# Performance work log

Hardware: AMD Instinct MI355X
Metric: run time of the kernel (lower is better)

## Reference

```python
import jax, jax.numpy as jnp
import numpy as np

N_QUBITS = 14
N_LAYERS = 2          # n_ansatz_layers
N_TIMESTEPS = 4
DEGREE = 2
N_ROTS = 4 * N_QUBITS * N_LAYERS  # 448 rotation params per qnode call
DIM = 2 ** N_QUBITS
BSZ = 256
STATE_DIM = 4
OUT_DIM = 2


def apply_ry(state, wire, theta):
    # state: (B, 2^n) complex64; theta: (B,) float. Wire 0 = most significant bit (PennyLane convention).
    L, R = 2 ** wire, 2 ** (N_QUBITS - wire - 1)
    st = state.reshape(-1, L, 2, R)
    c = jnp.cos(theta * 0.5)[:, None, None]
    s = jnp.sin(theta * 0.5)[:, None, None]
    s0, s1 = st[:, :, 0, :], st[:, :, 1, :]
    new = jnp.stack([c * s0 - s * s1, s * s0 + c * s1], axis=2)
    return new.reshape(state.shape)


def apply_crx(state, ctrl, tgt, theta):
    # Controlled-RX: RX(theta) on tgt when ctrl bit is 1.
    a, b = (ctrl, tgt) if ctrl < tgt else (tgt, ctrl)
    La, Lm, Lr = 2 ** a, 2 ** (b - a - 1), 2 ** (N_QUBITS - b - 1)
    st = state.reshape(-1, La, 2, Lm, 2, Lr)
    c = jnp.cos(theta * 0.5)[:, None, None, None]
    s = jnp.sin(theta * 0.5)[:, None, None, None]
    if ctrl < tgt:
        # axis2 = ctrl, axis4 = tgt
        ctl1 = st[:, :, 1]                      # (B, La, Lm, 2, Lr)
        t0, t1 = ctl1[:, :, :, 0, :], ctl1[:, :, :, 1, :]
        n0 = c * t0 - 1j * s * t1
        n1 = -1j * s * t0 + c * t1
        new_ctl1 = jnp.stack([n0, n1], axis=3)
        out = jnp.stack([st[:, :, 0], new_ctl1], axis=2)
    else:
        # axis2 = tgt, axis4 = ctrl
        t0c1, t1c1 = st[:, :, 0, :, 1, :], st[:, :, 1, :, 1, :]
        n0 = c * t0c1 - 1j * s * t1c1
        n1 = -1j * s * t0c1 + c * t1c1
        new_t0 = jnp.stack([st[:, :, 0, :, 0, :], n0], axis=3)
        new_t1 = jnp.stack([st[:, :, 1, :, 0, :], n1], axis=3)
        out = jnp.stack([new_t0, new_t1], axis=2)
    return out.reshape(state.shape)


def sim14(state, params):
    # sim14_circuit: per layer -> RY ring, descending CRX ring [i,(i+1)%n], RY ring, CRX ring [i,(i-1)%n].
    idx = 0
    for _ in range(N_LAYERS):
        for i in range(N_QUBITS):
            state = apply_ry(state, i, params[:, idx]); idx += 1
        for i in range(N_QUBITS - 1, -1, -1):
            state = apply_crx(state, i, (i + 1) % N_QUBITS, params[:, idx]); idx += 1
        for i in range(N_QUBITS):
            state = apply_ry(state, i, params[:, idx]); idx += 1
        for i in [N_QUBITS - 1] + list(range(N_QUBITS - 1)):
            state = apply_crx(state, i, (i - 1) % N_QUBITS, params[:, idx]); idx += 1
    return state


def poly_state(base, tparams, mix_coeffs, poly_coeffs):
    # evaluate_polynomial_state_pl: degree+1 rounds of timestep-mixed circuit outputs.
    result = jnp.zeros_like(base)
    for d in range(DEGREE + 1):
        mixed = jnp.zeros_like(base)
        for t in range(N_TIMESTEPS):
            mixed = mixed + mix_coeffs[:, t:t + 1] * sim14(base, tparams[:, t, :])
        result = result + poly_coeffs[d] * mixed
        if d < DEGREE:
            nrm = jnp.linalg.norm(mixed, axis=1, keepdims=True)
            base = mixed / (nrm + 1e-9)
    return result


def expval_z(state, wire):
    L, R = 2 ** wire, 2 ** (N_QUBITS - wire - 1)
    st = state.reshape(-1, L, 2, R)
    p = jnp.sum(jnp.abs(st) ** 2, axis=(1, 3))  # (B, 2)
    return p[:, 0] - p[:, 1]


def setup_inputs() -> dict:
    key = jax.random.key(0)
    ks = jax.random.split(key, 7)
    return {
        "x": jax.random.normal(ks[0], (BSZ, STATE_DIM), dtype=jnp.float32),
        "W_in": jax.random.normal(ks[1], (STATE_DIM, N_TIMESTEPS * N_ROTS), dtype=jnp.float32) * 0.3,
        "b_in": jax.random.normal(ks[2], (N_TIMESTEPS * N_ROTS,), dtype=jnp.float32) * 0.1,
        "mix_coeffs": jax.random.normal(ks[3], (1, N_TIMESTEPS), dtype=jnp.float32) * 0.5,
        "poly_coeffs": jax.random.normal(ks[4], (DEGREE + 1,), dtype=jnp.float32) * 0.5,
        "W_out": jax.random.normal(ks[5], (N_QUBITS, OUT_DIM), dtype=jnp.float32) * 0.3,
        "b_out": jax.random.normal(ks[6], (OUT_DIM,), dtype=jnp.float32) * 0.1,
    }


def reference(x, W_in, b_in, mix_coeffs, poly_coeffs, W_out, b_out):
    bsz = x.shape[0]
    # v1-style sigmoid [0,1] angle scaling
    angles = jax.nn.sigmoid(x @ W_in + b_in)                # (B, T*n_rots)
    tparams = angles.reshape(bsz, N_TIMESTEPS, N_ROTS)
    base = jnp.zeros((bsz, DIM), dtype=jnp.complex64).at[:, 0].set(1.0)
    final = poly_state(base, tparams, mix_coeffs, poly_coeffs)
    final = final / (jnp.linalg.norm(final, axis=1, keepdims=True) + 1e-9)
    expz = jnp.stack([expval_z(final, w) for w in range(N_QUBITS)], axis=1)  # (B, n_qubits) real
    return expz.astype(jnp.float32) @ W_out + b_out
```

## Files before the change

### kernel.cpp

```cpp
#include <hip/hip_runtime.h>
#include <math.h>

#define DIM 16384
#define NTH 512

typedef float v2f __attribute__((ext_vector_type(2)));

__host__ __device__ constexpr int cswz(int i) {
  return i ^ ((i >> 4) & 15) ^ ((i >> 8) & 15) ^ ((i >> 12) & 3);
}

constexpr int LW[8][5] = {
  {13, 12, 11, 10, 0},
  {10, 9, 8, 7, 6},
  {6, 5, 4, 3, 2},
  {2, 1, 0, 3, 4},
  {12, 13, 0, 1, 2},
  {2, 3, 4, 5, 6},
  {6, 7, 8, 9, 10},
  {10, 11, 12, 13, 9},
};
constexpr int PMAP[8][9] = {
  {4, 5, 6, 7, 8, 9, 10, 11, 12},
  {0, 1, 2, 11, 8, 9, 10, 12, 13},
  {0, 1, 2, 3, 4, 5, 6, 12, 13},
  {0, 1, 2, 3, 4, 5, 6, 7, 8},
  {2, 3, 4, 5, 6, 7, 8, 9, 10},
  {0, 1, 2, 3, 4, 5, 6, 12, 13},
  {0, 1, 2, 11, 8, 9, 10, 12, 13},
  {5, 6, 7, 8, 9, 10, 11, 12, 13},
};
constexpr int NG[8] = {9, 8, 8, 3, 9, 8, 8, 3};
constexpr int GATES[8][9][4] = {
  {{0,4,0,0},{0,3,0,10},{0,2,0,11},{0,1,0,12},{0,0,0,13},{1,0,4,14},{1,1,0,15},{1,2,1,16},{1,3,2,17}},
  {{0,4,0,6},{0,3,0,7},{0,2,0,8},{0,1,0,9},{1,1,0,18},{1,2,1,19},{1,3,2,20},{1,4,3,21},{0,0,0,0}},
  {{0,4,0,2},{0,3,0,3},{0,2,0,4},{0,1,0,5},{1,1,0,22},{1,2,1,23},{1,3,2,24},{1,4,3,25},{0,0,0,0}},
  {{0,1,0,1},{1,1,0,26},{1,2,1,27},{0,0,0,0},{0,0,0,0},{0,0,0,0},{0,0,0,0},{0,0,0,0},{0,0,0,0}},
  {{0,2,0,28},{0,3,0,29},{0,4,0,30},{0,0,0,40},{0,1,0,41},{1,1,0,42},{1,2,1,43},{1,3,2,44},{1,4,3,45}},
  {{0,1,0,31},{0,2,0,32},{0,3,0,33},{0,4,0,34},{1,1,0,46},{1,2,1,47},{1,3,2,48},{1,4,3,49},{0,0,0,0}},
  {{0,1,0,35},{0,2,0,36},{0,3,0,37},{0,4,0,38},{1,1,0,50},{1,2,1,51},{1,3,2,52},{1,4,3,53},{0,0,0,0}},
  {{0,1,0,39},{1,1,0,54},{1,2,1,55},{0,0,0,0},{0,0,0,0},{0,0,0,0},{0,0,0,0},{0,0,0,0},{0,0,0,0}},
};

__host__ __device__ constexpr int offcube(int p, int j) {
  int o = 0;
  for (int b = 0; b < 5; ++b)
    if ((j >> b) & 1) o |= 1 << (13 - LW[p][b]);
  return o;
}

template <int PID, int MODE>
__device__ __forceinline__ void run_pass(v2f* __restrict__ S, const v2f* __restrict__ CS,
                                         int lb, int tid, v2f* __restrict__ a) {
  int base = 0;
#pragma unroll
  for (int k = 0; k < 9; ++k) base |= ((tid >> k) & 1) << PMAP[PID][k];
  const int sb = cswz(base);
  if (MODE == 1) {
#pragma unroll
    for (int j = 0; j < 32; ++j) a[j] = v2f{0.f, 0.f};
    if (tid == 0) a[0] = v2f{1.f, 0.f};
  } else {
#pragma unroll
    for (int j = 0; j < 32; ++j) a[j] = S[sb ^ cswz(offcube(PID, j))];
  }
#pragma unroll
  for (int g = 0; g < NG[PID]; ++g) {
    const v2f cs2 = CS[lb + GATES[PID][g][3]];
    const float c = cs2.x, s = cs2.y;
    if (GATES[PID][g][0] == 0) {
      const int tb = GATES[PID][g][1];
#pragma unroll
      for (int j = 0; j < 32; ++j)
        if (!((j >> tb) & 1)) {
          const int j2 = j | (1 << tb);
          const v2f a0 = a[j], a1 = a[j2];
          a[j]  = c * a0 - s * a1;
          a[j2] = s * a0 + c * a1;
        }
    } else {
      const int bc = GATES[PID][g][1], bt = GATES[PID][g][2];
#pragma unroll
      for (int j = 0; j < 32; ++j)
        if (((j >> bc) & 1) && !((j >> bt) & 1)) {
          const int j2 = j | (1 << bt);
          const v2f t0 = a[j], t1 = a[j2];
          a[j]  = c * t0 + s * v2f{t1.y, -t1.x};
          a[j2] = c * t1 + s * v2f{t0.y, -t0.x};
        }
    }
  }
  if (MODE != 2) {
#pragma unroll
    for (int j = 0; j < 32; ++j) S[sb ^ cswz(offcube(PID, j))] = a[j];
  }
  __syncthreads();
}

__device__ __forceinline__ void run_sim(v2f* __restrict__ S, const v2f* __restrict__ CS,
                                        int tid, v2f* __restrict__ a,
                                        const v2f* __restrict__ basev, int own_sb,
                                        bool initzero) {
  if (initzero) {
    run_pass<0, 1>(S, CS, 0, tid, a);
  } else {
#pragma unroll
    for (int j = 0; j < 32; ++j) S[own_sb ^ cswz(offcube(7, j))] = basev[j];
    __syncthreads();
    run_pass<0, 0>(S, CS, 0, tid, a);
  }
  run_pass<1, 0>(S, CS, 0, tid, a);
  run_pass<2, 0>(S, CS, 0, tid, a);
  run_pass<3, 0>(S, CS, 0, tid, a);
  run_pass<4, 0>(S, CS, 0, tid, a);
  run_pass<5, 0>(S, CS, 0, tid, a);
  run_pass<6, 0>(S, CS, 0, tid, a);
  run_pass<7, 0>(S, CS, 0, tid, a);
  run_pass<0, 0>(S, CS, 56, tid, a);
  run_pass<1, 0>(S, CS, 56, tid, a);
  run_pass<2, 0>(S, CS, 56, tid, a);
  run_pass<3, 0>(S, CS, 56, tid, a);
  run_pass<4, 0>(S, CS, 56, tid, a);
  run_pass<5, 0>(S, CS, 56, tid, a);
  run_pass<6, 0>(S, CS, 56, tid, a);
  run_pass<7, 2>(S, CS, 56, tid, a);
}

__device__ __forceinline__ float block_sum(float v, int tid, float* red) {
#pragma unroll
  for (int off = 32; off; off >>= 1) v += __shfl_xor(v, off);
  if ((tid & 63) == 0) red[tid >> 6] = v;
  __syncthreads();
  float tot = 0.f;
#pragma unroll
  for (int w = 0; w < 8; ++w) tot += red[w];
  __syncthreads();
  return tot;
}

__global__ void
__attribute__((amdgpu_flat_work_group_size(512, 512)))
__attribute__((amdgpu_waves_per_eu(2, 2)))
qts_kernel(
    const float* __restrict__ x, const float* __restrict__ Win,
    const float* __restrict__ bin, const float* __restrict__ mix,
    const float* __restrict__ poly, const float* __restrict__ Wout,
    const float* __restrict__ bout, float* __restrict__ out) {
  extern __shared__ v2f S[];
  v2f* CSall = S + DIM;
  float* red = (float*)(S + DIM + 448);
  const int tid = threadIdx.x;
  const int b = blockIdx.x;

  if (tid < 448) {
    float z = bin[tid];
    const float x0 = x[b * 4 + 0], x1 = x[b * 4 + 1], x2 = x[b * 4 + 2], x3 = x[b * 4 + 3];
    z += x0 * Win[tid] + x1 * Win[448 + tid] + x2 * Win[896 + tid] + x3 * Win[1344 + tid];
    const float th = 1.f / (1.f + expf(-z));
    float sn, cc;
    sincosf(0.5f * th, &sn, &cc);
    CSall[tid] = v2f{cc, sn};
  }
  __syncthreads();

  int ownbase = 0;
#pragma unroll
  for (int k = 0; k < 9; ++k) ownbase |= ((tid >> k) & 1) << PMAP[7][k];
  const int own_sb = cswz(ownbase);

  const float p0 = poly[0], p1 = poly[1], p2 = poly[2];

  v2f a[32], acc[32], basev[32];
  float alpha;

#pragma unroll
  for (int j = 0; j < 32; ++j) acc[j] = v2f{0.f, 0.f};
  for (int t = 0; t < 4; ++t) {
    run_sim(S, CSall + t * 112, tid, a, basev, own_sb, true);
    const float mc = mix[t];
#pragma unroll
    for (int j = 0; j < 32; ++j) acc[j] += mc * a[j];
  }
  {
    float part = 0.f;
#pragma unroll
    for (int j = 0; j < 32; ++j) part += acc[j].x * acc[j].x + acc[j].y * acc[j].y;
    const float tot = block_sum(part, tid, red);
    const float nu = sqrtf(tot) + 1e-9f;
    const float inv = 1.f / nu;
    alpha = p0 * nu;
#pragma unroll
    for (int j = 0; j < 32; ++j) { basev[j] = inv * acc[j]; acc[j] = v2f{0.f, 0.f}; }
  }

  for (int t = 0; t < 4; ++t) {
    run_sim(S, CSall + t * 112, tid, a, basev, own_sb, false);
    const float mc = mix[t];
#pragma unroll
    for (int j = 0; j < 32; ++j) acc[j] += mc * a[j];
  }
  {
    float part = 0.f;
#pragma unroll
    for (int j = 0; j < 32; ++j) part += acc[j].x * acc[j].x + acc[j].y * acc[j].y;
    const float tot = block_sum(part, tid, red);
    const float nu = sqrtf(tot) + 1e-9f;
    const float inv = 1.f / nu;
#pragma unroll
    for (int j = 0; j < 32; ++j) {
      const v2f tmp = acc[j];
      acc[j] = alpha * basev[j] + p1 * tmp;
      basev[j] = inv * tmp;
    }
  }

  for (int t = 0; t < 4; ++t) {
    run_sim(S, CSall + t * 112, tid, a, basev, own_sb, false);
    const float mc = p2 * mix[t];
#pragma unroll
    for (int j = 0; j < 32; ++j) acc[j] += mc * a[j];
  }

  float part[15];
#pragma unroll
  for (int v = 0; v < 15; ++v) part[v] = 0.f;
#pragma unroll
  for (int j = 0; j < 32; ++j) {
    const int idx = ownbase | offcube(7, j);
    const float p = acc[j].x * acc[j].x + acc[j].y * acc[j].y;
    part[14] += p;
#pragma unroll
    for (int w = 0; w < 14; ++w) part[w] += ((idx >> (13 - w)) & 1) ? -p : p;
  }
  __syncthreads();
#pragma unroll
  for (int v = 0; v < 15; ++v) {
    float xv = part[v];
#pragma unroll
    for (int off = 32; off; off >>= 1) xv += __shfl_xor(xv, off);
    if ((tid & 63) == 0) red[(tid >> 6) * 15 + v] = xv;
  }
  __syncthreads();
  if (tid < 15) {
    float tot = 0.f;
#pragma unroll
    for (int w = 0; w < 8; ++w) tot += red[w * 15 + tid];
    red[128 + tid] = tot;
  }
  __syncthreads();
  if (tid < 2) {
    const float nrm = sqrtf(red[128 + 14]) + 1e-9f;
    const float iv = 1.f / (nrm * nrm);
    float o = bout[tid];
#pragma unroll
    for (int w = 0; w < 14; ++w) o += red[128 + w] * iv * Wout[w * 2 + tid];
    out[b * 2 + tid] = o;
  }
}

extern "C" void kernel_launch(void* const* d_in, const int* in_sizes, int n_in,
                              void* d_out, int out_size, void* d_ws, size_t ws_size,
                              hipStream_t stream) {
  const float* x    = (const float*)d_in[0];
  const float* Win  = (const float*)d_in[1];
  const float* bin  = (const float*)d_in[2];
  const float* mix  = (const float*)d_in[3];
  const float* poly = (const float*)d_in[4];
  const float* Wout = (const float*)d_in[5];
  const float* bout = (const float*)d_in[6];
  float* out = (float*)d_out;

  const size_t shmem = (size_t)DIM * sizeof(v2f) + 448 * sizeof(v2f) + 1024;
  hipFuncSetAttribute((const void*)qts_kernel,
                      hipFuncAttributeMaxDynamicSharedMemorySize, (int)shmem);
  qts_kernel<<<256, NTH, shmem, stream>>>(x, Win, bin, mix, poly, Wout, bout, out);
}
```

Baseline: 945.7 us.

## Use 1024 threads with 16 amplitudes each and a 10-pass gate schedule

The block grows from 512 to 1024 threads. Each thread now holds 16 amplitudes over a 4-qubit local subcube instead of 32 over 5 qubits, and the gate schedule is regrouped into 10 passes per layer instead of 8. Per-pass base offsets are precomputed once into a register array. The aim is to cut register pressure and raise the number of waves hiding LDS latency, at the cost of more shared-memory passes and __syncthreads barriers per simulation.

```diff
diff --git a/kernel.cpp b/kernel.cpp
--- a/kernel.cpp
+++ b/kernel.cpp
@@ -2,7 +2,8 @@
 #include <math.h>
 
 #define DIM 16384
-#define NTH 512
+#define NTH 1024
+#define APT 16
 
 typedef float v2f __attribute__((ext_vector_type(2)));
 
@@ -10,68 +11,70 @@
   return i ^ ((i >> 4) & 15) ^ ((i >> 8) & 15) ^ ((i >> 12) & 3);
 }
 
-constexpr int LW[8][5] = {
-  {13, 12, 11, 10, 0},
-  {10, 9, 8, 7, 6},
-  {6, 5, 4, 3, 2},
-  {2, 1, 0, 3, 4},
-  {12, 13, 0, 1, 2},
-  {2, 3, 4, 5, 6},
-  {6, 7, 8, 9, 10},
-  {10, 11, 12, 13, 9},
+constexpr int LWp[10][4] = {
+  {13, 0, 12, 11},
+  {10, 9, 8, 11},
+  {7, 6, 5, 8},
+  {4, 3, 2, 5},
+  {1, 0, 2, 3},
+  {13, 12, 0, 1},
+  {2, 1, 3, 4},
+  {5, 4, 6, 7},
+  {8, 7, 9, 10},
+  {11, 10, 12, 9},
 };
-constexpr int PMAP[8][9] = {
-  {4, 5, 6, 7, 8, 9, 10, 11, 12},
-  {0, 1, 2, 11, 8, 9, 10, 12, 13},
-  {0, 1, 2, 3, 4, 5, 6, 12, 13},
-  {0, 1, 2, 3, 4, 5, 6, 7, 8},
-  {2, 3, 4, 5, 6, 7, 8, 9, 10},
-  {0, 1, 2, 3, 4, 5, 6, 12, 13},
-  {0, 1, 2, 11, 8, 9, 10, 12, 13},
-  {5, 6, 7, 8, 9, 10, 11, 12, 13},
+constexpr int PM[10][10] = {
+  {3, 4, 5, 6, 7, 8, 9, 10, 11, 12},
+  {0, 1, 6, 7, 8, 9, 10, 11, 12, 13},
+  {0, 1, 2, 3, 4, 9, 10, 11, 12, 13},
+  {0, 1, 2, 3, 4, 5, 6, 7, 12, 13},
+  {0, 1, 2, 3, 4, 5, 6, 7, 8, 9},
+  {2, 3, 4, 5, 6, 7, 8, 9, 10, 11},
+  {0, 1, 2, 3, 4, 5, 6, 7, 8, 13},
+  {0, 1, 2, 3, 4, 5, 10, 11, 12, 13},
+  {0, 1, 2, 7, 8, 9, 10, 11, 12, 13},
+  {0, 5, 6, 7, 8, 9, 10, 11, 12, 13},
 };
-constexpr int NG[8] = {9, 8, 8, 3, 9, 8, 8, 3};
-constexpr int GATES[8][9][4] = {
-  {{0,4,0,0},{0,3,0,10},{0,2,0,11},{0,1,0,12},{0,0,0,13},{1,0,4,14},{1,1,0,15},{1,2,1,16},{1,3,2,17}},
-  {{0,4,0,6},{0,3,0,7},{0,2,0,8},{0,1,0,9},{1,1,0,18},{1,2,1,19},{1,3,2,20},{1,4,3,21},{0,0,0,0}},
-  {{0,4,0,2},{0,3,0,3},{0,2,0,4},{0,1,0,5},{1,1,0,22},{1,2,1,23},{1,3,2,24},{1,4,3,25},{0,0,0,0}},
-  {{0,1,0,1},{1,1,0,26},{1,2,1,27},{0,0,0,0},{0,0,0,0},{0,0,0,0},{0,0,0,0},{0,0,0,0},{0,0,0,0}},
-  {{0,2,0,28},{0,3,0,29},{0,4,0,30},{0,0,0,40},{0,1,0,41},{1,1,0,42},{1,2,1,43},{1,3,2,44},{1,4,3,45}},
-  {{0,1,0,31},{0,2,0,32},{0,3,0,33},{0,4,0,34},{1,1,0,46},{1,2,1,47},{1,3,2,48},{1,4,3,49},{0,0,0,0}},
-  {{0,1,0,35},{0,2,0,36},{0,3,0,37},{0,4,0,38},{1,1,0,50},{1,2,1,51},{1,3,2,52},{1,4,3,53},{0,0,0,0}},
-  {{0,1,0,39},{1,1,0,54},{1,2,1,55},{0,0,0,0},{0,0,0,0},{0,0,0,0},{0,0,0,0},{0,0,0,0},{0,0,0,0}},
+constexpr int NGp[10] = {7, 6, 6, 6, 3, 7, 6, 6, 6, 3};
+constexpr int GT[10][7][4] = {
+  {{0,0,0,13},{0,1,0,0},{0,2,0,12},{0,3,0,11},{1,0,1,14},{1,2,0,15},{1,3,2,16}},
+  {{0,0,0,10},{0,1,0,9},{0,2,0,8},{1,0,3,17},{1,1,0,18},{1,2,1,19},{0,0,0,0}},
+  {{0,0,0,7},{0,1,0,6},{0,2,0,5},{1,0,3,20},{1,1,0,21},{1,2,1,22},{0,0,0,0}},
+  {{0,0,0,4},{0,1,0,3},{0,2,0,2},{1,0,3,23},{1,1,0,24},{1,2,1,25},{0,0,0,0}},
+  {{0,0,0,1},{1,0,2,26},{1,1,0,27},{0,0,0,0},{0,0,0,0},{0,0,0,0},{0,0,0,0}},
+  {{0,0,0,41},{0,1,0,40},{0,2,0,28},{0,3,0,29},{1,0,1,42},{1,2,0,43},{1,3,2,44}},
+  {{0,0,0,30},{0,2,0,31},{0,3,0,32},{1,0,1,45},{1,2,0,46},{1,3,2,47},{0,0,0,0}},
+  {{0,0,0,33},{0,2,0,34},{0,3,0,35},{1,0,1,48},{1,2,0,49},{1,3,2,50},{0,0,0,0}},
+  {{0,0,0,36},{0,2,0,37},{0,3,0,38},{1,0,1,51},{1,2,0,52},{1,3,2,53},{0,0,0,0}},
+  {{0,0,0,39},{1,0,1,54},{1,2,0,55},{0,0,0,0},{0,0,0,0},{0,0,0,0},{0,0,0,0}},
 };
 
 __host__ __device__ constexpr int offcube(int p, int j) {
   int o = 0;
-  for (int b = 0; b < 5; ++b)
-    if ((j >> b) & 1) o |= 1 << (13 - LW[p][b]);
+  for (int b = 0; b < 4; ++b)
+    if ((j >> b) & 1) o |= 1 << (13 - LWp[p][b]);
   return o;
 }
 
 template <int PID, int MODE>
 __device__ __forceinline__ void run_pass(v2f* __restrict__ S, const v2f* __restrict__ CS,
-                                         int lb, int tid, v2f* __restrict__ a) {
-  int base = 0;
-#pragma unroll
-  for (int k = 0; k < 9; ++k) base |= ((tid >> k) & 1) << PMAP[PID][k];
-  const int sb = cswz(base);
+                                         int sb, int tid, v2f* __restrict__ a) {
   if (MODE == 1) {
 #pragma unroll
-    for (int j = 0; j < 32; ++j) a[j] = v2f{0.f, 0.f};
+    for (int j = 0; j < APT; ++j) a[j] = v2f{0.f, 0.f};
     if (tid == 0) a[0] = v2f{1.f, 0.f};
   } else {
 #pragma unroll
-    for (int j = 0; j < 32; ++j) a[j] = S[sb ^ cswz(offcube(PID, j))];
-  }
-#pragma unroll
-  for (int g = 0; g < NG[PID]; ++g) {
-    const v2f cs2 = CS[lb + GATES[PID][g][3]];
+    for (int j = 0; j < APT; ++j) a[j] = S[sb ^ cswz(offcube(PID, j))];
+  }
+#pragma unroll
+  for (int g = 0; g < NGp[PID]; ++g) {
+    const v2f cs2 = CS[GT[PID][g][3]];
     const float c = cs2.x, s = cs2.y;
-    if (GATES[PID][g][0] == 0) {
-      const int tb = GATES[PID][g][1];
-#pragma unroll
-      for (int j = 0; j < 32; ++j)
+    if (GT[PID][g][0] == 0) {
+      const int tb = GT[PID][g][1];
+#pragma unroll
+      for (int j = 0; j < APT; ++j)
         if (!((j >> tb) & 1)) {
           const int j2 = j | (1 << tb);
           const v2f a0 = a[j], a1 = a[j2];
@@ -79,9 +82,9 @@
           a[j2] = s * a0 + c * a1;
         }
     } else {
-      const int bc = GATES[PID][g][1], bt = GATES[PID][g][2];
-#pragma unroll
-      for (int j = 0; j < 32; ++j)
+      const int bc = GT[PID][g][1], bt = GT[PID][g][2];
+#pragma unroll
+      for (int j = 0; j < APT; ++j)
         if (((j >> bc) & 1) && !((j >> bt) & 1)) {
           const int j2 = j | (1 << bt);
           const v2f t0 = a[j], t1 = a[j2];
@@ -92,38 +95,44 @@
   }
   if (MODE != 2) {
 #pragma unroll
-    for (int j = 0; j < 32; ++j) S[sb ^ cswz(offcube(PID, j))] = a[j];
-  }
-  __syncthreads();
-}
-
+    for (int j = 0; j < APT; ++j) S[sb ^ cswz(offcube(PID, j))] = a[j];
+  }
+  __syncthreads();
+}
+
+template <bool INIT>
 __device__ __forceinline__ void run_sim(v2f* __restrict__ S, const v2f* __restrict__ CS,
                                         int tid, v2f* __restrict__ a,
-                                        const v2f* __restrict__ basev, int own_sb,
-                                        bool initzero) {
-  if (initzero) {
-    run_pass<0, 1>(S, CS, 0, tid, a);
+                                        const v2f* __restrict__ basev,
+                                        const int* __restrict__ sbv) {
+  if (INIT) {
+    run_pass<0, 1>(S, CS, sbv[0], tid, a);
   } else {
 #pragma unroll
-    for (int j = 0; j < 32; ++j) S[own_sb ^ cswz(offcube(7, j))] = basev[j];
+    for (int j = 0; j < APT; ++j) S[sbv[9] ^ cswz(offcube(9, j))] = basev[j];
     __syncthreads();
-    run_pass<0, 0>(S, CS, 0, tid, a);
-  }
-  run_pass<1, 0>(S, CS, 0, tid, a);
-  run_pass<2, 0>(S, CS, 0, tid, a);
-  run_pass<3, 0>(S, CS, 0, tid, a);
-  run_pass<4, 0>(S, CS, 0, tid, a);
-  run_pass<5, 0>(S, CS, 0, tid, a);
-  run_pass<6, 0>(S, CS, 0, tid, a);
-  run_pass<7, 0>(S, CS, 0, tid, a);
-  run_pass<0, 0>(S, CS, 56, tid, a);
-  run_pass<1, 0>(S, CS, 56, tid, a);
-  run_pass<2, 0>(S, CS, 56, tid, a);
-  run_pass<3, 0>(S, CS, 56, tid, a);
-  run_pass<4, 0>(S, CS, 56, tid, a);
-  run_pass<5, 0>(S, CS, 56, tid, a);
-  run_pass<6, 0>(S, CS, 56, tid, a);
-  run_pass<7, 2>(S, CS, 56, tid, a);
+    run_pass<0, 0>(S, CS, sbv[0], tid, a);
+  }
+  run_pass<1, 0>(S, CS, sbv[1], tid, a);
+  run_pass<2, 0>(S, CS, sbv[2], tid, a);
+  run_pass<3, 0>(S, CS, sbv[3], tid, a);
+  run_pass<4, 0>(S, CS, sbv[4], tid, a);
+  run_pass<5, 0>(S, CS, sbv[5], tid, a);
+  run_pass<6, 0>(S, CS, sbv[6], tid, a);
+  run_pass<7, 0>(S, CS, sbv[7], tid, a);
+  run_pass<8, 0>(S, CS, sbv[8], tid, a);
+  run_pass<9, 0>(S, CS, sbv[9], tid, a);
+  const v2f* C2 = CS + 56;
+  run_pass<0, 0>(S, C2, sbv[0], tid, a);
+  run_pass<1, 0>(S, C2, sbv[1], tid, a);
+  run_pass<2, 0>(S, C2, sbv[2], tid, a);
+  run_pass<3, 0>(S, C2, sbv[3], tid, a);
+  run_pass<4, 0>(S, C2, sbv[4], tid, a);
+  run_pass<5, 0>(S, C2, sbv[5], tid, a);
+  run_pass<6, 0>(S, C2, sbv[6], tid, a);
+  run_pass<7, 0>(S, C2, sbv[7], tid, a);
+  run_pass<8, 0>(S, C2, sbv[8], tid, a);
+  run_pass<9, 2>(S, C2, sbv[9], tid, a);
 }
 
 __device__ __forceinline__ float block_sum(float v, int tid, float* red) {
@@ -133,15 +142,12 @@
   __syncthreads();
   float tot = 0.f;
 #pragma unroll
-  for (int w = 0; w < 8; ++w) tot += red[w];
+  for (int w = 0; w < NTH / 64; ++w) tot += red[w];
   __syncthreads();
   return tot;
 }
 
-__global__ void
-__attribute__((amdgpu_flat_work_group_size(512, 512)))
-__attribute__((amdgpu_waves_per_eu(2, 2)))
-qts_kernel(
+__global__ __launch_bounds__(NTH, 4) void qts_kernel(
     const float* __restrict__ x, const float* __restrict__ Win,
     const float* __restrict__ bin, const float* __restrict__ mix,
     const float* __restrict__ poly, const float* __restrict__ Wout,
@@ -163,51 +169,58 @@
   }
   __syncthreads();
 
+  int sbv[10];
+#pragma unroll
+  for (int p = 0; p < 10; ++p) {
+    int base = 0;
+#pragma unroll
+    for (int k = 0; k < 10; ++k) base |= ((tid >> k) & 1) << PM[p][k];
+    sbv[p] = cswz(base);
+  }
   int ownbase = 0;
 #pragma unroll
-  for (int k = 0; k < 9; ++k) ownbase |= ((tid >> k) & 1) << PMAP[7][k];
-  const int own_sb = cswz(ownbase);
+  for (int k = 0; k < 10; ++k) ownbase |= ((tid >> k) & 1) << PM[9][k];
 
   const float p0 = poly[0], p1 = poly[1], p2 = poly[2];
 
-  v2f a[32], acc[32], basev[32];
+  v2f a[APT], acc[APT], basev[APT];
   float alpha;
 
 #pragma unroll
-  for (int j = 0; j < 32; ++j) acc[j] = v2f{0.f, 0.f};
+  for (int j = 0; j < APT; ++j) acc[j] = v2f{0.f, 0.f};
   for (int t = 0; t < 4; ++t) {
-    run_sim(S, CSall + t * 112, tid, a, basev, own_sb, true);
+    run_sim<true>(S, CSall + t * 112, tid, a, basev, sbv);
     const float mc = mix[t];
 #pragma unroll
-    for (int j = 0; j < 32; ++j) acc[j] += mc * a[j];
+    for (int j = 0; j < APT; ++j) acc[j] += mc * a[j];
   }
   {
     float part = 0.f;
 #pragma unroll
-    for (int j = 0; j < 32; ++j) part += acc[j].x * acc[j].x + acc[j].y * acc[j].y;
+    for (int j = 0; j < APT; ++j) part += acc[j].x * acc[j].x + acc[j].y * acc[j].y;
     const float tot = block_sum(part, tid, red);
     const float nu = sqrtf(tot) + 1e-9f;
     const float inv = 1.f / nu;
     alpha = p0 * nu;
 #pragma unroll
-    for (int j = 0; j < 32; ++j) { basev[j] = inv * acc[j]; acc[j] = v2f{0.f, 0.f}; }
+    for (int j = 0; j < APT; ++j) { basev[j] = inv * acc[j]; acc[j] = v2f{0.f, 0.f}; }
   }
 
   for (int t = 0; t < 4; ++t) {
-    run_sim(S, CSall + t * 112, tid, a, basev, own_sb, false);
+    run_sim<false>(S, CSall + t * 112, tid, a, basev, sbv);
     const float mc = mix[t];
 #pragma unroll
-    for (int j = 0; j < 32; ++j) acc[j] += mc * a[j];
+    for (int j = 0; j < APT; ++j) acc[j] += mc * a[j];
   }
   {
     float part = 0.f;
 #pragma unroll
-    for (int j = 0; j < 32; ++j) part += acc[j].x * acc[j].x + acc[j].y * acc[j].y;
+    for (int j = 0; j < APT; ++j) part += acc[j].x * acc[j].x + acc[j].y * acc[j].y;
     const float tot = block_sum(part, tid, red);
     const float nu = sqrtf(tot) + 1e-9f;
     const float inv = 1.f / nu;
 #pragma unroll
-    for (int j = 0; j < 32; ++j) {
+    for (int j = 0; j < APT; ++j) {
       const v2f tmp = acc[j];
       acc[j] = alpha * basev[j] + p1 * tmp;
       basev[j] = inv * tmp;
@@ -215,18 +228,18 @@
   }
 
   for (int t = 0; t < 4; ++t) {
-    run_sim(S, CSall + t * 112, tid, a, basev, own_sb, false);
+    run_sim<false>(S, CSall + t * 112, tid, a, basev, sbv);
     const float mc = p2 * mix[t];
 #pragma unroll
-    for (int j = 0; j < 32; ++j) acc[j] += mc * a[j];
+    for (int j = 0; j < APT; ++j) acc[j] += mc * a[j];
   }
 
   float part[15];
 #pragma unroll
   for (int v = 0; v < 15; ++v) part[v] = 0.f;
 #pragma unroll
-  for (int j = 0; j < 32; ++j) {
-    const int idx = ownbase | offcube(7, j);
+  for (int j = 0; j < APT; ++j) {
+    const int idx = ownbase | offcube(9, j);
     const float p = acc[j].x * acc[j].x + acc[j].y * acc[j].y;
     part[14] += p;
 #pragma unroll
@@ -244,16 +257,16 @@
   if (tid < 15) {
     float tot = 0.f;
 #pragma unroll
-    for (int w = 0; w < 8; ++w) tot += red[w * 15 + tid];
-    red[128 + tid] = tot;
+    for (int w = 0; w < NTH / 64; ++w) tot += red[w * 15 + tid];
+    red[240 + tid] = tot;
   }
   __syncthreads();
   if (tid < 2) {
-    const float nrm = sqrtf(red[128 + 14]) + 1e-9f;
+    const float nrm = sqrtf(red[240 + 14]) + 1e-9f;
     const float iv = 1.f / (nrm * nrm);
     float o = bout[tid];
 #pragma unroll
-    for (int w = 0; w < 14; ++w) o += red[128 + w] * iv * Wout[w * 2 + tid];
+    for (int w = 0; w < 14; ++w) o += red[240 + w] * iv * Wout[w * 2 + tid];
     out[b * 2 + tid] = o;
   }
 }
```

Measured after the change: 982.2 us. 1.04x slower.
